# Kernel tuning notes

Hardware: AMD Instinct MI355X
Metric: run time of the kernel (lower is better)

The kernel has to match this reference:

```python
import jax, jax.numpy as jnp
import numpy as np

H = 8      # heads
DK = 64    # k_size
DV = 128   # output_size // heads
DIN = 1024 # input_size


def setup_inputs() -> dict:
    key = jax.random.key(0)
    ks = jax.random.split(key, 10)
    B, C = 4, 2048
    p = lambda k, sh: jax.random.normal(k, sh, jnp.float32) * 0.02
    return {
        "x": jax.random.normal(ks[0], (B, C, DIN), jnp.float32),
        "mask": jax.random.normal(ks[1], (B, C), jnp.float32),
        "Mq_w": p(ks[2], (H * DK, DIN)), "Mq_b": p(ks[3], (H * DK,)),
        "Mk_w": p(ks[4], (H * DK, DIN)), "Mk_b": p(ks[5], (H * DK,)),
        "Mv_w": p(ks[6], (H * DV, DIN)), "Mv_b": p(ks[7], (H * DV,)),
        "Wo_w": p(ks[8], (H * DV, H * DV)), "Wo_b": p(ks[9], (H * DV,)),
    }


def reference(x, mask, Mq_w, Mq_b, Mk_w, Mk_b, Mv_w, Mv_b, Wo_w, Wo_b):
    B, C, _ = x.shape
    # torch .view(B, heads, C, -1) on a [B, C, H*D] tensor is a FLAT reshape
    # (not a transpose) -- replicated here verbatim.
    q = (x @ Mq_w.T + Mq_b).reshape(B, H, C, DK)
    k = (x @ Mk_w.T + Mk_b).reshape(B, H, C, DK)
    v = (x @ Mv_w.T + Mv_b).reshape(B, H, C, DV)
    scores = jnp.einsum('bhqd,bhkd->bhqk', q, k)            # [B,H,C,C]
    # mask is added per-QUERY position (unsqueeze(-1)), before the 1/sqrt(dk) scale
    scores = scores + mask[:, None, :, None]
    # original softmaxes over dim=1 of [B*H, C, C] == the query axis (axis=2 here)
    att = jax.nn.softmax(scores / jnp.sqrt(jnp.float32(DK)), axis=2)
    out = jnp.einsum('bhqk,bhkd->bhqd', att, v)              # [B,H,C,DV]
    out = out.reshape(B, C, H * DV)                          # flat reshape, as in .view(B, C, -1)
    return out @ Wo_w.T + Wo_b
```

## Files before the change

### kernel.cpp

```cpp
#include <hip/hip_runtime.h>
#include <cstdint>
#include <cstddef>

constexpr int Cc = 2048;
constexpr int Mrows = 8192;

typedef __attribute__((ext_vector_type(8))) short short8;
typedef __attribute__((ext_vector_type(4))) float floatx4;
typedef __attribute__((ext_vector_type(4))) unsigned short ushortx4;
typedef unsigned short us;

#define MFMA_BF16(a, b, c) __builtin_amdgcn_mfma_f32_16x16x32_bf16((a), (b), (c), 0, 0, 0)

__device__ __forceinline__ us f2bf(float f) {
  union { float f; unsigned u; } v; v.f = f;
  unsigned r = v.u + 0x7fffu + ((v.u >> 16) & 1u);
  return (us)(r >> 16);
}
__device__ __forceinline__ float bf2f(us u) {
  union { unsigned u; float f; } v; v.u = ((unsigned)u) << 16;
  return v.f;
}
__device__ __forceinline__ void async16(const us* g, us* l) {
  __builtin_amdgcn_global_load_lds(
      (const __attribute__((address_space(1))) unsigned int*)(g),
      (__attribute__((address_space(3))) unsigned int*)(l), 16, 0, 0);
}

__global__ __launch_bounds__(256) void cast_all(
    const float* __restrict__ x,  const float* __restrict__ mq,
    const float* __restrict__ mk, const float* __restrict__ mv,
    const float* __restrict__ wo,
    us* __restrict__ xb, us* __restrict__ wqb, us* __restrict__ wkb,
    us* __restrict__ wvb, us* __restrict__ wob)
{
  size_t i = ((size_t)blockIdx.x * 256 + threadIdx.x) * 8;
  const float* src; us* dst; size_t j;
  if      (i <  8388608) { src = x;  dst = xb;  j = i; }
  else if (i <  8912896) { src = mq; dst = wqb; j = i -  8388608; }
  else if (i <  9437184) { src = mk; dst = wkb; j = i -  8912896; }
  else if (i < 10485760) { src = mv; dst = wvb; j = i -  9437184; }
  else if (i < 11534336) { src = wo; dst = wob; j = i - 10485760; }
  else return;
  float4 a = *(const float4*)(src + j);
  float4 b = *(const float4*)(src + j + 4);
  short8 o;
  o[0] = (short)f2bf(a.x); o[1] = (short)f2bf(a.y);
  o[2] = (short)f2bf(a.z); o[3] = (short)f2bf(a.w);
  o[4] = (short)f2bf(b.x); o[5] = (short)f2bf(b.y);
  o[6] = (short)f2bf(b.z); o[7] = (short)f2bf(b.w);
  *(short8*)(dst + j) = o;
}

template<int OUT_BF16>
__global__ __launch_bounds__(256) void gemm_mfma(
    const us* __restrict__ A, const us* __restrict__ W,
    const float* __restrict__ bias, void* __restrict__ outp,
    int M, int N, int K)
{
  __shared__ __align__(16) us As[128 * 64];
  __shared__ __align__(16) us Ws[128 * 64];
  const int t = threadIdx.x, lane = t & 63, wid = t >> 6;
  const int wr = wid >> 1, wc = wid & 1;
  const int quad = lane >> 4, l15 = lane & 15, l7 = l15 & 7;
  const int m0 = blockIdx.y * 128, n0 = blockIdx.x * 128;

  floatx4 acc[4][4];
#pragma unroll
  for (int i = 0; i < 4; i++)
#pragma unroll
    for (int j = 0; j < 4; j++) acc[i][j] = (floatx4){0.f, 0.f, 0.f, 0.f};

  for (int k0 = 0; k0 < K; k0 += 64) {
    __syncthreads();
#pragma unroll
    for (int j = 0; j < 4; j++) {
      int f = (wid * 4 + j) * 64 + lane;
      int row = f >> 3, sc = (f & 7) ^ (row & 7);
      async16(A + (size_t)(m0 + row) * K + k0 + sc * 8, &As[f * 8]);
      async16(W + (size_t)(n0 + row) * K + k0 + sc * 8, &Ws[f * 8]);
    }
    __syncthreads();
    short8 aF[4][2], bF[4][2];
#pragma unroll
    for (int fm = 0; fm < 4; fm++) {
      int ra = wr * 64 + fm * 16 + l15;
      int rb = wc * 64 + fm * 16 + l15;
#pragma unroll
      for (int c = 0; c < 2; c++) {
        aF[fm][c] = *(const short8*)&As[ra * 64 + (((c << 2) + quad) ^ l7) * 8];
        bF[fm][c] = *(const short8*)&Ws[rb * 64 + (((c << 2) + quad) ^ l7) * 8];
      }
    }
#pragma unroll
    for (int i = 0; i < 4; i++)
#pragma unroll
      for (int j = 0; j < 4; j++) {
        floatx4 d = MFMA_BF16(aF[i][0], bF[j][0], acc[i][j]);
        acc[i][j] = MFMA_BF16(aF[i][1], bF[j][1], d);
      }
  }

#pragma unroll
  for (int fn = 0; fn < 4; fn++) {
    int col = n0 + wc * 64 + fn * 16 + l15;
    float bv = bias[col];
#pragma unroll
    for (int fm = 0; fm < 4; fm++) {
#pragma unroll
      for (int r = 0; r < 4; r++) {
        int m = m0 + wr * 64 + fm * 16 + quad * 4 + r;
        float v = acc[fm][fn][r] + bv;
        if (OUT_BF16)
          ((us*)outp)[(size_t)m * N + col] = f2bf(v);
        else
          ((float*)outp)[(size_t)m * N + col] = v;
      }
    }
  }
}

__global__ __launch_bounds__(256, 2) void attn_pass1(
    const us* __restrict__ Q_, const us* __restrict__ K_,
    const float* __restrict__ mask, float* __restrict__ invZ)
{
  __shared__ __align__(16) us Qs[2][128 * 64];
  const int t = threadIdx.x, lane = t & 63, wid = t >> 6;
  const int quad = lane >> 4, l15 = lane & 15, l7 = l15 & 7;
  const int bh = blockIdx.y, b = bh >> 3;
  const int kt = blockIdx.x * 128;
  const us* Kb = K_ + (size_t)bh * Cc * 64;
  const us* Qb = Q_ + (size_t)bh * Cc * 64;
  const float* mrow = mask + (size_t)b * Cc;

  short8 kA[2][2];
#pragma unroll
  for (int kf = 0; kf < 2; kf++)
#pragma unroll
    for (int c = 0; c < 2; c++)
      kA[kf][c] = *(const short8*)(Kb + (size_t)(kt + wid * 32 + kf * 16 + l15) * 64 + c * 32 + quad * 8);

  float zacc[2][4] = {};

#pragma unroll
  for (int j = 0; j < 4; j++) {
    int f = (wid * 4 + j) * 64 + lane;
    int row = f >> 3, sc = (f & 7) ^ (row & 7);
    async16(Qb + (size_t)row * 64 + sc * 8, &Qs[0][f * 8]);
  }
  __syncthreads();

  int p = 0;
  for (int it = 0; it < 16; it++) {
    if (it + 1 < 16) {
#pragma unroll
      for (int j = 0; j < 4; j++) {
        int f = (wid * 4 + j) * 64 + lane;
        int row = f >> 3, sc = (f & 7) ^ (row & 7);
        async16(Qb + (size_t)((it + 1) * 128 + row) * 64 + sc * 8, &Qs[1 - p][f * 8]);
      }
    }
    const us* Qsp = Qs[p];
#pragma unroll
    for (int qf = 0; qf < 8; qf++) {
      int row = qf * 16 + l15;
      short8 q0 = *(const short8*)&Qsp[row * 64 + ((quad) ^ l7) * 8];
      short8 q1 = *(const short8*)&Qsp[row * 64 + ((4 + quad) ^ l7) * 8];
      float mv = mrow[it * 128 + qf * 16 + l15] * 0.125f;
#pragma unroll
      for (int kf = 0; kf < 2; kf++) {
        floatx4 d = (floatx4){0.f, 0.f, 0.f, 0.f};
        d = MFMA_BF16(kA[kf][0], q0, d);
        d = MFMA_BF16(kA[kf][1], q1, d);
#pragma unroll
        for (int r = 0; r < 4; r++)
          zacc[kf][r] += __expf(fmaf(d[r], 0.125f, mv));
      }
    }
    __syncthreads();
    p ^= 1;
  }

#pragma unroll
  for (int kf = 0; kf < 2; kf++)
#pragma unroll
    for (int r = 0; r < 4; r++) {
      float v = zacc[kf][r];
      v += __shfl_xor(v, 1); v += __shfl_xor(v, 2);
      v += __shfl_xor(v, 4); v += __shfl_xor(v, 8);
      if (l15 == 0)
        invZ[(size_t)bh * Cc + kt + wid * 32 + kf * 16 + quad * 4 + r] = 1.0f / v;
    }
}

__global__ __launch_bounds__(256) void transpose_v(
    const us* __restrict__ V, const float* __restrict__ invZ,
    us* __restrict__ VT)
{
  __shared__ __align__(16) us Vs[32][136];
  __shared__ float izs[32];
  const int bh = blockIdx.y, ct = blockIdx.x * 32;
  const int t = threadIdx.x;
  const us* Vb  = V  + (size_t)bh * Cc * 128;
  us*       VTb = VT + (size_t)bh * 128 * Cc;
#pragma unroll
  for (int i = 0; i < 2; i++) {
    int idx = t + i * 256, c = idx >> 4, d0 = (idx & 15) * 8;
    *(short8*)&Vs[c][d0] = *(const short8*)(Vb + (size_t)(ct + c) * 128 + d0);
  }
  if (t < 32) izs[t] = invZ[(size_t)bh * Cc + ct + t];
  __syncthreads();
#pragma unroll
  for (int i = 0; i < 2; i++) {
    int idx = t + i * 256, dv = idx >> 2, cb = (idx & 3) * 8;
    short8 o;
#pragma unroll
    for (int j = 0; j < 8; j++)
      o[j] = (short)f2bf(bf2f(Vs[cb + j][dv]) * izs[cb + j]);
    *(short8*)(VTb + (size_t)dv * Cc + ct + cb) = o;
  }
}

__global__ __launch_bounds__(256, 2) void attn_pass2(
    const us* __restrict__ Q_, const us* __restrict__ K_,
    const us* __restrict__ VT_, const float* __restrict__ mask,
    us* __restrict__ Ab)
{
  __shared__ __align__(16) us Ks[2][64 * 64];
  __shared__ __align__(16) us VTs[2][128 * 64];
  __shared__ __align__(16) us Ps[128 * 64];
  const int t = threadIdx.x, lane = t & 63, wid = t >> 6;
  const int quad = lane >> 4, l15 = lane & 15, l7 = l15 & 7;
  const int bh = blockIdx.y, b = bh >> 3;
  const int qt = blockIdx.x * 128;
  const us* Qb  = Q_  + (size_t)bh * Cc * 64;
  const us* Kb  = K_  + (size_t)bh * Cc * 64;
  const us* VTb = VT_ + (size_t)bh * 128 * Cc;

  short8 qB[2][2];
  float mvs[2];
#pragma unroll
  for (int qf = 0; qf < 2; qf++) {
    int q = qt + wid * 32 + qf * 16 + l15;
#pragma unroll
    for (int c = 0; c < 2; c++)
      qB[qf][c] = *(const short8*)(Qb + (size_t)q * 64 + c * 32 + quad * 8);
    mvs[qf] = mask[(size_t)b * Cc + q] * 0.125f;
  }

  floatx4 acc[2][8];
#pragma unroll
  for (int qf = 0; qf < 2; qf++)
#pragma unroll
    for (int fn = 0; fn < 8; fn++) acc[qf][fn] = (floatx4){0.f, 0.f, 0.f, 0.f};

#pragma unroll
  for (int j = 0; j < 2; j++) {
    int f = (wid * 2 + j) * 64 + lane;
    int row = f >> 3, sc = (f & 7) ^ (row & 7);
    async16(Kb + (size_t)row * 64 + sc * 8, &Ks[0][f * 8]);
  }
#pragma unroll
  for (int j = 0; j < 4; j++) {
    int f = (wid * 4 + j) * 64 + lane;
    int row = f >> 3, sc = (f & 7) ^ (row & 7);
    async16(VTb + (size_t)row * Cc + sc * 8, &VTs[0][f * 8]);
  }
  __syncthreads();

  int p = 0;
  for (int kb = 0; kb < Cc; kb += 64) {
    if (kb + 64 < Cc) {
#pragma unroll
      for (int j = 0; j < 2; j++) {
        int f = (wid * 2 + j) * 64 + lane;
        int row = f >> 3, sc = (f & 7) ^ (row & 7);
        async16(Kb + (size_t)(kb + 64 + row) * 64 + sc * 8, &Ks[1 - p][f * 8]);
      }
#pragma unroll
      for (int j = 0; j < 4; j++) {
        int f = (wid * 4 + j) * 64 + lane;
        int row = f >> 3, sc = (f & 7) ^ (row & 7);
        async16(VTb + (size_t)row * Cc + kb + 64 + sc * 8, &VTs[1 - p][f * 8]);
      }
    }
    const us* Ksp = Ks[p];
    const us* Vsp = VTs[p];

    short8 kA[4][2];
#pragma unroll
    for (int kf = 0; kf < 4; kf++) {
      int row = kf * 16 + l15;
#pragma unroll
      for (int c = 0; c < 2; c++)
        kA[kf][c] = *(const short8*)&Ksp[row * 64 + (((c << 2) + quad) ^ l7) * 8];
    }
#pragma unroll
    for (int kf = 0; kf < 4; kf++) {
#pragma unroll
      for (int qf = 0; qf < 2; qf++) {
        floatx4 d = (floatx4){0.f, 0.f, 0.f, 0.f};
        d = MFMA_BF16(kA[kf][0], qB[qf][0], d);
        d = MFMA_BF16(kA[kf][1], qB[qf][1], d);
        ushortx4 pk;
#pragma unroll
        for (int r = 0; r < 4; r++)
          pk[r] = f2bf(__expf(fmaf(d[r], 0.125f, mvs[qf])));
        int prow = wid * 32 + qf * 16 + l15;
        *(ushortx4*)&Ps[prow * 64 + (((kf << 1) + (quad >> 1)) ^ l7) * 8 + (quad & 1) * 4] = pk;
      }
    }

    short8 pA[2][2];
#pragma unroll
    for (int qf = 0; qf < 2; qf++) {
      int prow = wid * 32 + qf * 16 + l15;
#pragma unroll
      for (int kc = 0; kc < 2; kc++)
        pA[qf][kc] = *(const short8*)&Ps[prow * 64 + (((kc << 2) + quad) ^ l7) * 8];
    }
#pragma unroll
    for (int fn = 0; fn < 8; fn++) {
      int vrow = fn * 16 + l15;
#pragma unroll
      for (int kc = 0; kc < 2; kc++) {
        short8 vB = *(const short8*)&Vsp[vrow * 64 + (((kc << 2) + quad) ^ l7) * 8];
#pragma unroll
        for (int qf = 0; qf < 2; qf++)
          acc[qf][fn] = MFMA_BF16(pA[qf][kc], vB, acc[qf][fn]);
      }
    }
    __syncthreads();
    p ^= 1;
  }

#pragma unroll
  for (int qf = 0; qf < 2; qf++)
#pragma unroll
    for (int fn = 0; fn < 8; fn++)
#pragma unroll
      for (int r = 0; r < 4; r++) {
        int q = qt + wid * 32 + qf * 16 + quad * 4 + r;
        Ab[((size_t)bh * Cc + q) * 128 + fn * 16 + l15] = f2bf(acc[qf][fn][r]);
      }
}

extern "C" void kernel_launch(void* const* d_in, const int* in_sizes, int n_in,
                              void* d_out, int out_size, void* d_ws, size_t ws_size,
                              hipStream_t stream)
{
  const float* x    = (const float*)d_in[0];
  const float* mask = (const float*)d_in[1];
  const float* Mq_w = (const float*)d_in[2];
  const float* Mq_b = (const float*)d_in[3];
  const float* Mk_w = (const float*)d_in[4];
  const float* Mk_b = (const float*)d_in[5];
  const float* Mv_w = (const float*)d_in[6];
  const float* Mv_b = (const float*)d_in[7];
  const float* Wo_w = (const float*)d_in[8];
  const float* Wo_b = (const float*)d_in[9];
  float* outp = (float*)d_out;

  us* xb  = (us*)d_ws;
  us* wq  = xb  + 8388608;
  us* wk  = wq  + 524288;
  us* wv  = wk  + 524288;
  us* wo  = wv  + 1048576;
  us* Qb  = wo  + 1048576;
  us* Kb  = Qb  + 4194304;
  us* Vb  = Kb  + 4194304;
  us* VTb = Vb  + 8388608;
  us* Ab  = VTb + 8388608;
  float* invZ = (float*)(Ab + 8388608);

  dim3 blk(256);
  cast_all<<<5632, blk, 0, stream>>>(x, Mq_w, Mk_w, Mv_w, Wo_w, xb, wq, wk, wv, wo);

  gemm_mfma<1><<<dim3(4, 64), blk, 0, stream>>>(xb, wq, Mq_b, Qb, Mrows, 512, 1024);
  gemm_mfma<1><<<dim3(4, 64), blk, 0, stream>>>(xb, wk, Mk_b, Kb, Mrows, 512, 1024);
  gemm_mfma<1><<<dim3(8, 64), blk, 0, stream>>>(xb, wv, Mv_b, Vb, Mrows, 1024, 1024);

  attn_pass1<<<dim3(16, 32), blk, 0, stream>>>(Qb, Kb, mask, invZ);
  transpose_v<<<dim3(64, 32), blk, 0, stream>>>(Vb, invZ, VTb);
  attn_pass2<<<dim3(16, 32), blk, 0, stream>>>(Qb, Kb, VTb, mask, Ab);

  gemm_mfma<0><<<dim3(8, 64), blk, 0, stream>>>(Ab, wo, Wo_b, outp, Mrows, 1024, 1024);
}
```

Baseline: 317.1 us.

## Fuse QKV GEMMs, remap grids, use exp2, restructure attention pass2 pipeline

Merges the three projection GEMMs into one launch over the contiguous concatenated weight buffer, with block-id swizzles in the GEMM and attention kernels. Switches exp to exp2 with a folded log2e scale and packs bf16 conversions through the HIP bf16 intrinsics. Pass2 is restructured: K fragments are loaded straight from global into registers, the P tile is double-buffered so the next tile's QK^T/exp overlaps the current PV, and waves are split differently between the score and PV phases. This aims to cut launch count and improve overlap and L2 locality, at the cost of more registers and reliance on wq/wk/wv being adjacent in the workspace.

```diff
diff --git a/kernel.cpp b/kernel.cpp
--- a/kernel.cpp
+++ b/kernel.cpp
@@ -1,16 +1,18 @@
 #include <hip/hip_runtime.h>
+#include <hip/hip_bf16.h>
 #include <cstdint>
 #include <cstddef>
 
 constexpr int Cc = 2048;
 constexpr int Mrows = 8192;
+constexpr float SC2 = 0.18033688011112042f;
 
 typedef __attribute__((ext_vector_type(8))) short short8;
 typedef __attribute__((ext_vector_type(4))) float floatx4;
-typedef __attribute__((ext_vector_type(4))) unsigned short ushortx4;
 typedef unsigned short us;
 
 #define MFMA_BF16(a, b, c) __builtin_amdgcn_mfma_f32_16x16x32_bf16((a), (b), (c), 0, 0, 0)
+#define EXP2F(x) __builtin_amdgcn_exp2f(x)
 
 __device__ __forceinline__ us f2bf(float f) {
   union { float f; unsigned u; } v; v.f = f;
@@ -20,6 +22,12 @@
 __device__ __forceinline__ float bf2f(us u) {
   union { unsigned u; float f; } v; v.u = ((unsigned)u) << 16;
   return v.f;
+}
+__device__ __forceinline__ uint2 pack4bf(float e0, float e1, float e2, float e3) {
+  union { __hip_bfloat162 h; unsigned u; } a, b;
+  a.h = __float22bfloat162_rn(float2{e0, e1});
+  b.h = __float22bfloat162_rn(float2{e2, e3});
+  return uint2{a.u, b.u};
 }
 __device__ __forceinline__ void async16(const us* g, us* l) {
   __builtin_amdgcn_global_load_lds(
@@ -52,18 +60,90 @@
   *(short8*)(dst + j) = o;
 }
 
-template<int OUT_BF16>
-__global__ __launch_bounds__(256) void gemm_mfma(
-    const us* __restrict__ A, const us* __restrict__ W,
-    const float* __restrict__ bias, void* __restrict__ outp,
-    int M, int N, int K)
+__global__ __launch_bounds__(256, 3) void gemm_qkv(
+    const us* __restrict__ A, const us* __restrict__ Wall,
+    const float* __restrict__ bq, const float* __restrict__ bk,
+    const float* __restrict__ bv,
+    us* __restrict__ Qo, us* __restrict__ Ko, us* __restrict__ Vo)
 {
   __shared__ __align__(16) us As[128 * 64];
   __shared__ __align__(16) us Ws[128 * 64];
   const int t = threadIdx.x, lane = t & 63, wid = t >> 6;
   const int wr = wid >> 1, wc = wid & 1;
   const int quad = lane >> 4, l15 = lane & 15, l7 = l15 & 7;
-  const int m0 = blockIdx.y * 128, n0 = blockIdx.x * 128;
+  const int id = blockIdx.x;
+  const int nt = (id & 7) * 2 + ((id >> 3) & 1);
+  const int mt = id >> 4;
+  const int m0 = mt * 128, n0 = nt * 128;
+  const int K = 1024;
+
+  floatx4 acc[4][4];
+#pragma unroll
+  for (int i = 0; i < 4; i++)
+#pragma unroll
+    for (int j = 0; j < 4; j++) acc[i][j] = (floatx4){0.f, 0.f, 0.f, 0.f};
+
+  for (int k0 = 0; k0 < K; k0 += 64) {
+    __syncthreads();
+#pragma unroll
+    for (int j = 0; j < 4; j++) {
+      int f = (wid * 4 + j) * 64 + lane;
+      int row = f >> 3, sc = (f & 7) ^ (row & 7);
+      async16(A    + (size_t)(m0 + row) * K + k0 + sc * 8, &As[f * 8]);
+      async16(Wall + (size_t)(n0 + row) * K + k0 + sc * 8, &Ws[f * 8]);
+    }
+    __syncthreads();
+    short8 aF[4][2], bF[4][2];
+#pragma unroll
+    for (int fm = 0; fm < 4; fm++) {
+      int ra = wr * 64 + fm * 16 + l15;
+      int rb = wc * 64 + fm * 16 + l15;
+#pragma unroll
+      for (int c = 0; c < 2; c++) {
+        aF[fm][c] = *(const short8*)&As[ra * 64 + (((c << 2) + quad) ^ l7) * 8];
+        bF[fm][c] = *(const short8*)&Ws[rb * 64 + (((c << 2) + quad) ^ l7) * 8];
+      }
+    }
+#pragma unroll
+    for (int i = 0; i < 4; i++)
+#pragma unroll
+      for (int j = 0; j < 4; j++) {
+        floatx4 d = MFMA_BF16(aF[i][0], bF[j][0], acc[i][j]);
+        acc[i][j] = MFMA_BF16(aF[i][1], bF[j][1], d);
+      }
+  }
+
+  us* dst; const float* bias; int Nout, c0;
+  if (nt < 4)      { dst = Qo; bias = bq; Nout = 512;  c0 = n0; }
+  else if (nt < 8) { dst = Ko; bias = bk; Nout = 512;  c0 = n0 - 512; }
+  else             { dst = Vo; bias = bv; Nout = 1024; c0 = n0 - 1024; }
+
+#pragma unroll
+  for (int fn = 0; fn < 4; fn++) {
+    int col = c0 + wc * 64 + fn * 16 + l15;
+    float bvv = bias[col];
+#pragma unroll
+    for (int fm = 0; fm < 4; fm++)
+#pragma unroll
+      for (int r = 0; r < 4; r++) {
+        int m = m0 + wr * 64 + fm * 16 + quad * 4 + r;
+        dst[(size_t)m * Nout + col] = f2bf(acc[fm][fn][r] + bvv);
+      }
+  }
+}
+
+__global__ __launch_bounds__(256, 3) void gemm_out(
+    const us* __restrict__ A, const us* __restrict__ W,
+    const float* __restrict__ bias, float* __restrict__ outp)
+{
+  __shared__ __align__(16) us As[128 * 64];
+  __shared__ __align__(16) us Ws[128 * 64];
+  const int t = threadIdx.x, lane = t & 63, wid = t >> 6;
+  const int wr = wid >> 1, wc = wid & 1;
+  const int quad = lane >> 4, l15 = lane & 15, l7 = l15 & 7;
+  const int id = blockIdx.x;
+  const int m0 = (id >> 3) * 128, n0 = (id & 7) * 128;
+  const int K = 1024, N = 1024;
 
   floatx4 acc[4][4];
 #pragma unroll
@@ -104,19 +184,14 @@
 #pragma unroll
   for (int fn = 0; fn < 4; fn++) {
     int col = n0 + wc * 64 + fn * 16 + l15;
-    float bv = bias[col];
-#pragma unroll
-    for (int fm = 0; fm < 4; fm++) {
+    float bvv = bias[col];
+#pragma unroll
+    for (int fm = 0; fm < 4; fm++)
 #pragma unroll
       for (int r = 0; r < 4; r++) {
         int m = m0 + wr * 64 + fm * 16 + quad * 4 + r;
-        float v = acc[fm][fn][r] + bv;
-        if (OUT_BF16)
-          ((us*)outp)[(size_t)m * N + col] = f2bf(v);
-        else
-          ((float*)outp)[(size_t)m * N + col] = v;
-      }
-    }
+        outp[(size_t)m * N + col] = acc[fm][fn][r] + bvv;
+      }
   }
 }
 
@@ -127,8 +202,10 @@
   __shared__ __align__(16) us Qs[2][128 * 64];
   const int t = threadIdx.x, lane = t & 63, wid = t >> 6;
   const int quad = lane >> 4, l15 = lane & 15, l7 = l15 & 7;
-  const int bh = blockIdx.y, b = bh >> 3;
-  const int kt = blockIdx.x * 128;
+  const int id = blockIdx.x;
+  const int bh = (id & 7) * 4 + ((id >> 3) & 3);
+  const int kt = (id >> 5) * 128;
+  const int b = bh >> 3;
   const us* Kb = K_ + (size_t)bh * Cc * 64;
   const us* Qb = Q_ + (size_t)bh * Cc * 64;
   const float* mrow = mask + (size_t)b * Cc;
@@ -166,7 +243,7 @@
       int row = qf * 16 + l15;
       short8 q0 = *(const short8*)&Qsp[row * 64 + ((quad) ^ l7) * 8];
       short8 q1 = *(const short8*)&Qsp[row * 64 + ((4 + quad) ^ l7) * 8];
-      float mv = mrow[it * 128 + qf * 16 + l15] * 0.125f;
+      float mv = mrow[it * 128 + qf * 16 + l15] * SC2;
 #pragma unroll
       for (int kf = 0; kf < 2; kf++) {
         floatx4 d = (floatx4){0.f, 0.f, 0.f, 0.f};
@@ -174,7 +251,7 @@
         d = MFMA_BF16(kA[kf][1], q1, d);
 #pragma unroll
         for (int r = 0; r < 4; r++)
-          zacc[kf][r] += __expf(fmaf(d[r], 0.125f, mv));
+          zacc[kf][r] += EXP2F(fmaf(d[r], SC2, mv));
       }
     }
     __syncthreads();
@@ -226,122 +303,141 @@
     const us* __restrict__ VT_, const float* __restrict__ mask,
     us* __restrict__ Ab)
 {
-  __shared__ __align__(16) us Ks[2][64 * 64];
   __shared__ __align__(16) us VTs[2][128 * 64];
-  __shared__ __align__(16) us Ps[128 * 64];
+  __shared__ __align__(16) us Ps[2][128 * 64];
   const int t = threadIdx.x, lane = t & 63, wid = t >> 6;
   const int quad = lane >> 4, l15 = lane & 15, l7 = l15 & 7;
-  const int bh = blockIdx.y, b = bh >> 3;
-  const int qt = blockIdx.x * 128;
+  const int id = blockIdx.x;
+  const int bh = (id & 7) * 4 + ((id >> 3) & 3);
+  const int qt = (id >> 5) * 128;
+  const int b = bh >> 3;
   const us* Qb  = Q_  + (size_t)bh * Cc * 64;
   const us* Kb  = K_  + (size_t)bh * Cc * 64;
   const us* VTb = VT_ + (size_t)bh * 128 * Cc;
 
-  short8 qB[2][2];
-  float mvs[2];
-#pragma unroll
-  for (int qf = 0; qf < 2; qf++) {
-    int q = qt + wid * 32 + qf * 16 + l15;
+  const int kHalf = wid & 1, qHalfS = wid >> 1;
+  const int qPV = wid & 1, dvPV = wid >> 1;
+
+  short8 qB[4][2];
+  float mv2[4];
+#pragma unroll
+  for (int qq = 0; qq < 4; qq++) {
+    int q = qt + qHalfS * 64 + qq * 16 + l15;
 #pragma unroll
     for (int c = 0; c < 2; c++)
-      qB[qf][c] = *(const short8*)(Qb + (size_t)q * 64 + c * 32 + quad * 8);
-    mvs[qf] = mask[(size_t)b * Cc + q] * 0.125f;
-  }
-
-  floatx4 acc[2][8];
-#pragma unroll
-  for (int qf = 0; qf < 2; qf++)
-#pragma unroll
-    for (int fn = 0; fn < 8; fn++) acc[qf][fn] = (floatx4){0.f, 0.f, 0.f, 0.f};
-
-#pragma unroll
-  for (int j = 0; j < 2; j++) {
-    int f = (wid * 2 + j) * 64 + lane;
-    int row = f >> 3, sc = (f & 7) ^ (row & 7);
-    async16(Kb + (size_t)row * 64 + sc * 8, &Ks[0][f * 8]);
-  }
+      qB[qq][c] = *(const short8*)(Qb + (size_t)q * 64 + c * 32 + quad * 8);
+    mv2[qq] = mask[(size_t)b * Cc + q] * SC2;
+  }
+
+  floatx4 acc[4][4];
+#pragma unroll
+  for (int i = 0; i < 4; i++)
+#pragma unroll
+    for (int j = 0; j < 4; j++) acc[i][j] = (floatx4){0.f, 0.f, 0.f, 0.f};
+
+  short8 kA[2][2];
+#pragma unroll
+  for (int kk = 0; kk < 2; kk++)
+#pragma unroll
+    for (int c = 0; c < 2; c++)
+      kA[kk][c] = *(const short8*)(Kb + (size_t)((kHalf * 2 + kk) * 16 + l15) * 64 + c * 32 + quad * 8);
+
 #pragma unroll
   for (int j = 0; j < 4; j++) {
     int f = (wid * 4 + j) * 64 + lane;
     int row = f >> 3, sc = (f & 7) ^ (row & 7);
     async16(VTb + (size_t)row * Cc + sc * 8, &VTs[0][f * 8]);
   }
+
+#pragma unroll
+  for (int kk = 0; kk < 2; kk++) {
+    int kf = kHalf * 2 + kk;
+#pragma unroll
+    for (int qq = 0; qq < 4; qq++) {
+      floatx4 d = (floatx4){0.f, 0.f, 0.f, 0.f};
+      d = MFMA_BF16(kA[kk][0], qB[qq][0], d);
+      d = MFMA_BF16(kA[kk][1], qB[qq][1], d);
+      uint2 pk = pack4bf(EXP2F(fmaf(d[0], SC2, mv2[qq])),
+                         EXP2F(fmaf(d[1], SC2, mv2[qq])),
+                         EXP2F(fmaf(d[2], SC2, mv2[qq])),
+                         EXP2F(fmaf(d[3], SC2, mv2[qq])));
+      int prow = qHalfS * 64 + qq * 16 + l15;
+      *(uint2*)&Ps[0][prow * 64 + (((kf << 1) + (quad >> 1)) ^ l7) * 8 + (quad & 1) * 4] = pk;
+    }
+  }
+#pragma unroll
+  for (int kk = 0; kk < 2; kk++)
+#pragma unroll
+    for (int c = 0; c < 2; c++)
+      kA[kk][c] = *(const short8*)(Kb + (size_t)(64 + (kHalf * 2 + kk) * 16 + l15) * 64 + c * 32 + quad * 8);
   __syncthreads();
 
-  int p = 0;
+  int p = 0, s = 0;
   for (int kb = 0; kb < Cc; kb += 64) {
     if (kb + 64 < Cc) {
-#pragma unroll
-      for (int j = 0; j < 2; j++) {
-        int f = (wid * 2 + j) * 64 + lane;
-        int row = f >> 3, sc = (f & 7) ^ (row & 7);
-        async16(Kb + (size_t)(kb + 64 + row) * 64 + sc * 8, &Ks[1 - p][f * 8]);
-      }
 #pragma unroll
       for (int j = 0; j < 4; j++) {
         int f = (wid * 4 + j) * 64 + lane;
         int row = f >> 3, sc = (f & 7) ^ (row & 7);
         async16(VTb + (size_t)row * Cc + kb + 64 + sc * 8, &VTs[1 - p][f * 8]);
       }
-    }
-    const us* Ksp = Ks[p];
-    const us* Vsp = VTs[p];
-
-    short8 kA[4][2];
-#pragma unroll
-    for (int kf = 0; kf < 4; kf++) {
-      int row = kf * 16 + l15;
-#pragma unroll
-      for (int c = 0; c < 2; c++)
-        kA[kf][c] = *(const short8*)&Ksp[row * 64 + (((c << 2) + quad) ^ l7) * 8];
-    }
-#pragma unroll
-    for (int kf = 0; kf < 4; kf++) {
-#pragma unroll
-      for (int qf = 0; qf < 2; qf++) {
-        floatx4 d = (floatx4){0.f, 0.f, 0.f, 0.f};
-        d = MFMA_BF16(kA[kf][0], qB[qf][0], d);
-        d = MFMA_BF16(kA[kf][1], qB[qf][1], d);
-        ushortx4 pk;
-#pragma unroll
-        for (int r = 0; r < 4; r++)
-          pk[r] = f2bf(__expf(fmaf(d[r], 0.125f, mvs[qf])));
-        int prow = wid * 32 + qf * 16 + l15;
-        *(ushortx4*)&Ps[prow * 64 + (((kf << 1) + (quad >> 1)) ^ l7) * 8 + (quad & 1) * 4] = pk;
-      }
-    }
-
-    short8 pA[2][2];
-#pragma unroll
-    for (int qf = 0; qf < 2; qf++) {
-      int prow = wid * 32 + qf * 16 + l15;
+#pragma unroll
+      for (int kk = 0; kk < 2; kk++) {
+        int kf = kHalf * 2 + kk;
+#pragma unroll
+        for (int qq = 0; qq < 4; qq++) {
+          floatx4 d = (floatx4){0.f, 0.f, 0.f, 0.f};
+          d = MFMA_BF16(kA[kk][0], qB[qq][0], d);
+          d = MFMA_BF16(kA[kk][1], qB[qq][1], d);
+          uint2 pk = pack4bf(EXP2F(fmaf(d[0], SC2, mv2[qq])),
+                             EXP2F(fmaf(d[1], SC2, mv2[qq])),
+                             EXP2F(fmaf(d[2], SC2, mv2[qq])),
+                             EXP2F(fmaf(d[3], SC2, mv2[qq])));
+          int prow = qHalfS * 64 + qq * 16 + l15;
+          *(uint2*)&Ps[1 - s][prow * 64 + (((kf << 1) + (quad >> 1)) ^ l7) * 8 + (quad & 1) * 4] = pk;
+        }
+      }
+      if (kb + 128 < Cc) {
+#pragma unroll
+        for (int kk = 0; kk < 2; kk++)
+#pragma unroll
+          for (int c = 0; c < 2; c++)
+            kA[kk][c] = *(const short8*)(Kb + (size_t)(kb + 128 + (kHalf * 2 + kk) * 16 + l15) * 64 + c * 32 + quad * 8);
+      }
+    }
+
+    short8 pA[4][2];
+#pragma unroll
+    for (int qq = 0; qq < 4; qq++) {
+      int prow = qPV * 64 + qq * 16 + l15;
 #pragma unroll
       for (int kc = 0; kc < 2; kc++)
-        pA[qf][kc] = *(const short8*)&Ps[prow * 64 + (((kc << 2) + quad) ^ l7) * 8];
-    }
-#pragma unroll
-    for (int fn = 0; fn < 8; fn++) {
-      int vrow = fn * 16 + l15;
+        pA[qq][kc] = *(const short8*)&Ps[s][prow * 64 + (((kc << 2) + quad) ^ l7) * 8];
+    }
+#pragma unroll
+    for (int fn = 0; fn < 4; fn++) {
+      int vrow = dvPV * 64 + fn * 16 + l15;
 #pragma unroll
       for (int kc = 0; kc < 2; kc++) {
-        short8 vB = *(const short8*)&Vsp[vrow * 64 + (((kc << 2) + quad) ^ l7) * 8];
-#pragma unroll
-        for (int qf = 0; qf < 2; qf++)
-          acc[qf][fn] = MFMA_BF16(pA[qf][kc], vB, acc[qf][fn]);
-      }
-    }
-    __syncthreads();
-    p ^= 1;
-  }
-
-#pragma unroll
-  for (int qf = 0; qf < 2; qf++)
-#pragma unroll
-    for (int fn = 0; fn < 8; fn++)
+        short8 vB = *(const short8*)&VTs[p][vrow * 64 + (((kc << 2) + quad) ^ l7) * 8];
+#pragma unroll
+        for (int qq = 0; qq < 4; qq++)
+          acc[qq][fn] = MFMA_BF16(pA[qq][kc], vB, acc[qq][fn]);
+      }
+    }
+    __syncthreads();
+    p ^= 1; s ^= 1;
+  }
+
+#pragma unroll
+  for (int qq = 0; qq < 4; qq++)
+#pragma unroll
+    for (int fn = 0; fn < 4; fn++)
 #pragma unroll
       for (int r = 0; r < 4; r++) {
-        int q = qt + wid * 32 + qf * 16 + quad * 4 + r;
-        Ab[((size_t)bh * Cc + q) * 128 + fn * 16 + l15] = f2bf(acc[qf][fn][r]);
+        int q = qt + qPV * 64 + qq * 16 + quad * 4 + r;
+        int dv = dvPV * 64 + fn * 16 + l15;
+        Ab[((size_t)bh * Cc + q) * 128 + dv] = f2bf(acc[qq][fn][r]);
       }
 }
 
@@ -373,16 +469,13 @@
   us* Ab  = VTb + 8388608;
   float* invZ = (float*)(Ab + 8388608);
 
-  dim3 blk(256);
-  cast_all<<<5632, blk, 0, stream>>>(x, Mq_w, Mk_w, Mv_w, Wo_w, xb, wq, wk, wv, wo);
-
-  gemm_mfma<1><<<dim3(4, 64), blk, 0, stream>>>(xb, wq, Mq_b, Qb, Mrows, 512, 1024);
-  gemm_mfma<1><<<dim3(4, 64), blk, 0, stream>>>(xb, wk, Mk_b, Kb, Mrows, 512, 1024);
-  gemm_mfma<1><<<dim3(8, 64), blk, 0, stream>>>(xb, wv, Mv_b, Vb, Mrows, 1024, 1024);
-
-  attn_pass1<<<dim3(16, 32), blk, 0, stream>>>(Qb, Kb, mask, invZ);
-  transpose_v<<<dim3(64, 32), blk, 0, stream>>>(Vb, invZ, VTb);
-  attn_pass2<<<dim3(16, 32), blk, 0, stream>>>(Qb, Kb, VTb, mask, Ab);
-
-  gemm_mfma<0><<<dim3(8, 64), blk, 0, stream>>>(Ab, wo, Wo_b, outp, Mrows, 1024, 1024);
-}
+  cast_all<<<5632, 256, 0, stream>>>(x, Mq_w, Mk_w, Mv_w, Wo_w, xb, wq, wk, wv, wo);
+
+  gemm_qkv<<<1024, 256, 0, stream>>>(xb, wq, Mq_b, Mk_b, Mv_b, Qb, Kb, Vb);
+
+  attn_pass1<<<512, 256, 0, stream>>>(Qb, Kb, mask, invZ);
+  transpose_v<<<dim3(64, 32), 256, 0, stream>>>(Vb, invZ, VTb);
+  attn_pass2<<<512, 256, 0, stream>>>(Qb, Kb, VTb, mask, Ab);
+
+  gemm_out<<<512, 256, 0, stream>>>(Ab, wo, Wo_b, outp);
+}
```

New measurement: 289.7 us. -8.7%, faster.
